# Optimization experiments

Hardware: AMD Instinct MI355X
Metric: run time of the kernel (lower is better)

Reference implementation:

```python
import jax, jax.numpy as jnp
import numpy as np

SR = 44100
PRE_EMPH = 0.97
FRAME_LEN = int(0.02 * SR)      # 882
FRAME_HOP = FRAME_LEN // 2      # 441
N_FFT = 2048
EPS = 1e-10


def setup_inputs() -> dict:
    key = jax.random.key(0)
    k1, k2 = jax.random.split(key)
    waveform = jax.random.normal(k1, (16, 441000), dtype=jnp.float32)
    # librosa mel filterbank is a fixed nonnegative (n_mels, n_fft//2+1) matrix;
    # a random surrogate keeps the math (dense matmul) identical.
    mel_filters = jax.random.uniform(k2, (60, N_FFT // 2 + 1), dtype=jnp.float32)
    return {"waveform": waveform, "mel_filters": mel_filters}


def _mfdwc(waveform, mel_filters):
    dt = waveform.dtype
    # pre-emphasis: y[0]=x[0], y[t]=x[t]-0.97*x[t-1]
    emph = jnp.concatenate(
        [waveform[:, :1], waveform[:, 1:] - PRE_EMPH * waveform[:, :-1]], axis=1)
    L = emph.shape[1]
    n_frames = 1 + (L - FRAME_LEN) // FRAME_HOP  # static
    idx = jnp.arange(n_frames)[:, None] * FRAME_HOP + jnp.arange(FRAME_LEN)[None, :]
    frames = emph[:, idx]                                   # (B, T, 882)
    window = jnp.asarray(np.hamming(FRAME_LEN), dtype=dt)   # (882,)
    windowed = frames * window
    spec = jnp.fft.rfft(windowed, n=N_FFT, axis=-1)         # (B, T, 1025) complex
    power = jnp.real(spec) ** 2 + jnp.imag(spec) ** 2       # |FFT|^2
    mel = jnp.einsum('mf,btf->btm', mel_filters, power)     # (B, T, 60)
    logmel = jnp.log(mel + EPS)
    # 1-level Haar DWT along mel axis (pywt convention, even length):
    # cA = (x_even + x_odd)/sqrt(2), cD = (x_even - x_odd)/sqrt(2)
    sq2 = jnp.sqrt(jnp.asarray(2.0, dt))
    x_even, x_odd = logmel[..., 0::2], logmel[..., 1::2]
    cA = (x_even + x_odd) / sq2                             # (B, T, 30)
    cD = (x_even - x_odd) / sq2                             # (B, T, 30)
    # delta (window=3, edge-padded): d[t] = a[clamp(t+1)] - a[clamp(t-1)]
    fwd = jnp.concatenate([cA[:, 1:], cA[:, -1:]], axis=1)
    bwd = jnp.concatenate([cA[:, :1], cA[:, :-1]], axis=1)
    delta = fwd - bwd
    feats = jnp.concatenate([cA, delta, cD], axis=-1)       # (B, T, 90)
    mean = jnp.mean(feats, axis=1)
    std = jnp.std(feats, axis=1, ddof=1)                    # torch.std unbiased
    return jnp.concatenate([mean, std], axis=1)             # (B, 180)


def reference(waveform, mel_filters):
    return _mfdwc(waveform, mel_filters)
```

## Files before the change

### kernel.cpp

```cpp
#include <hip/hip_runtime.h>
#include <hip/hip_bf16.h>
#include <math.h>

#define FRAME_LEN 882
#define FRAME_HOP 441
#define NFFT 2048
#define NFRAMES 999
#define NBATCH 16
#define NMEL 60
#define WAVE_LEN 441000
#define PRE_EMPH 0.97f
#define EPS 1e-10f
#define NROWS (NBATCH * NFRAMES)
#define NPANEL 999
#define KPAD 1056
#define NKC 33
#define PANEL_ELEMS (NKC * 512)
#define PANEL_BYTES (PANEL_ELEMS * 2)
#define PI_F 3.14159265358979323846f

#define PADI(i) ((i) + ((i) >> 4))

__device__ __forceinline__ int frag_off(int m, int k) {
  return ((k >> 5) * 512) | (((k >> 3) & 3) * 128) | (m * 8) | (k & 7);
}

typedef float vf2 __attribute__((ext_vector_type(2)));
__device__ __forceinline__ vf2 mkv(float x, float y){ vf2 r; r.x = x; r.y = y; return r; }
__device__ __forceinline__ vf2 cmul(vf2 a, vf2 b){ return a.xx * b + mkv(-a.y, a.y) * b.yx; }
__device__ __forceinline__ vf2 rotni(vf2 z){ return mkv(z.y, -z.x); }

__device__ __forceinline__ void dif_group16(vf2* x, vf2 t1, bool zerohi) {
  const vf2 C81 = mkv(0.9238795325f, -0.3826834324f);
  const vf2 C82 = mkv(0.7071067812f, -0.7071067812f);
  const vf2 C83 = mkv(0.3826834324f, -0.9238795325f);
  vf2 w0 = t1, w1 = cmul(t1, C81), w2 = cmul(t1, C82), w3 = cmul(t1, C83);
  vf2 ws1[8] = {w0, w1, w2, w3, rotni(w0), rotni(w1), rotni(w2), rotni(w3)};
  if (zerohi) {
#pragma unroll
    for (int k = 0; k < 8; ++k) x[k + 8] = cmul(x[k], ws1[k]);
  } else {
#pragma unroll
    for (int k = 0; k < 8; ++k) {
      vf2 u = x[k], v = x[k + 8];
      x[k] = u + v;
      x[k + 8] = cmul(u - v, ws1[k]);
    }
  }
  vf2 t2 = cmul(t1, t1);
  vf2 v1 = cmul(t2, C82);
  vf2 ws2[4] = {t2, v1, rotni(t2), rotni(v1)};
#pragma unroll
  for (int h = 0; h < 2; ++h) {
#pragma unroll
    for (int k = 0; k < 4; ++k) {
      vf2 u = x[h*8 + k], v = x[h*8 + k + 4];
      x[h*8 + k] = u + v;
      x[h*8 + k + 4] = cmul(u - v, ws2[k]);
    }
  }
  vf2 t4 = cmul(t2, t2);
  vf2 t4r = rotni(t4);
#pragma unroll
  for (int h = 0; h < 4; ++h) {
    vf2 a = x[h*4 + 0], b = x[h*4 + 2];
    x[h*4 + 0] = a + b; x[h*4 + 2] = cmul(a - b, t4);
    a = x[h*4 + 1]; b = x[h*4 + 3];
    x[h*4 + 1] = a + b; x[h*4 + 3] = cmul(a - b, t4r);
  }
  vf2 t8 = cmul(t4, t4);
#pragma unroll
  for (int j = 0; j < 8; ++j) {
    vf2 a = x[2*j], b = x[2*j + 1];
    x[2*j] = a + b; x[2*j + 1] = cmul(a - b, t8);
  }
}

__device__ __forceinline__ void dif8(vf2* y) {
  const vf2 c1 = mkv(0.7071067812f, -0.7071067812f);
  const vf2 c3 = mkv(-0.7071067812f, -0.7071067812f);
  vf2 u, v;
  u=y[0]; v=y[4]; y[0]=u+v; y[4]=u-v;
  u=y[1]; v=y[5]; y[1]=u+v; y[5]=cmul(u-v, c1);
  u=y[2]; v=y[6]; y[2]=u+v; y[6]=rotni(u-v);
  u=y[3]; v=y[7]; y[3]=u+v; y[7]=cmul(u-v, c3);
  u=y[0]; v=y[2]; y[0]=u+v; y[2]=u-v;
  u=y[1]; v=y[3]; y[1]=u+v; y[3]=rotni(u-v);
  u=y[4]; v=y[6]; y[4]=u+v; y[6]=u-v;
  u=y[5]; v=y[7]; y[5]=u+v; y[7]=rotni(u-v);
  u=y[0]; v=y[1]; y[0]=u+v; y[1]=u-v;
  u=y[2]; v=y[3]; y[2]=u+v; y[3]=u-v;
  u=y[4]; v=y[5]; y[4]=u+v; y[5]=u-v;
  u=y[6]; v=y[7]; y[6]=u+v; y[7]=u-v;
}

__global__ __launch_bounds__(256) void fft_pow_kernel(
    const float* __restrict__ wav, const float* __restrict__ filt,
    __hip_bfloat16* __restrict__ powrF, __hip_bfloat16* __restrict__ filtbF)
{
  __shared__ vf2 lds2[2][NFFT + (NFFT >> 4)];
  const int id = blockIdx.x;

  if (id >= 4000) {
    const int mm = id - 4000;
    __hip_bfloat16* qp = filtbF + (size_t)(mm >> 4) * PANEL_ELEMS;
    const int m = mm & 15;
    for (int k = threadIdx.x; k < KPAD; k += 256) {
      float v = (mm < NMEL && k < 1025) ? filt[mm * 1025 + k] : 0.f;
      qp[frag_off(m, k)] = __float2bfloat16(v);
    }
    return;
  }

  const int t   = threadIdx.x;
  const int fid = t >> 7;
  const int tt  = t & 127;
  vf2* lds = lds2[fid];

  const int P  = id * 2 + fid;
  const int b  = P & 15;
  const int t0 = 2 * (P >> 4), t1f = t0 + 1;
  const bool has1 = (t1f < NFRAMES);
  const float* w = wav + (size_t)b * WAVE_LEN;
  const int s0 = t0 * FRAME_HOP;
  int s1 = t1f * FRAME_HOP;
  if (s1 > WAVE_LEN - FRAME_LEN) s1 = WAVE_LEN - FRAME_LEN;

  vf2 x[16];
  {
    float sB, cB, sD, cD;
    __sincosf(6.283185307179586f * (float)tt / 881.0f, &sB, &cB);
    __sincosf(6.283185307179586f * 128.0f / 881.0f, &sD, &cD);
    vf2 cur  = mkv(cB, sB);
    vf2 step = mkv(cD, sD);
#pragma unroll
    for (int k = 0; k < 7; ++k) {
      int i = k * 128 + tt;
      float v1 = 0.f, v2 = 0.f;
      if (i < FRAME_LEN) {
        float win = 0.54f - 0.46f * cur.x;
        int s = s0 + i;
        float e1 = (s > 0) ? (w[s] - PRE_EMPH * w[s - 1]) : w[s];
        v1 = e1 * win;
        int ss = s1 + i;
        v2 = (w[ss] - PRE_EMPH * w[ss - 1]) * win;
      }
      x[k] = mkv(v1, v2);
      cur = cmul(cur, step);
    }
#pragma unroll
    for (int k = 7; k < 16; ++k) x[k] = mkv(0.f, 0.f);
  }

  {
    float sA, cA;
    __sincosf(-PI_F * (float)tt / 1024.0f, &sA, &cA);
    dif_group16(x, mkv(cA, sA), true);
  }
#pragma unroll
  for (int k = 0; k < 16; ++k) lds[PADI(k * 128 + tt)] = x[k];
  __syncthreads();

  {
    const int Q = tt >> 3, r = tt & 7;
    const int base = Q * 128 + r;
#pragma unroll
    for (int k = 0; k < 16; ++k) x[k] = lds[PADI(base + k * 8)];
    float sA, cA;
    __sincosf(-PI_F * (float)r / 64.0f, &sA, &cA);
    dif_group16(x, mkv(cA, sA), false);
#pragma unroll
    for (int k = 0; k < 16; ++k) lds[PADI(base + k * 8)] = x[k];
  }
  __syncthreads();

  {
    vf2 ya[8], yb[8];
#pragma unroll
    for (int j = 0; j < 8; ++j) {
      ya[j] = lds[PADI(16 * tt + j)];
      yb[j] = lds[PADI(16 * tt + 8 + j)];
    }
    dif8(ya);
    dif8(yb);
    __syncthreads();
    const int r7 = (int)(__brev((unsigned)tt) >> 25);
    const int RA[8] = {0, 8, 4, 12, 2, 10, 6, 14};
    const int RB[8] = {1, 9, 5, 13, 3, 11, 7, 15};
#pragma unroll
    for (int j = 0; j < 8; ++j) {
      lds[PADI(RA[j] * 128 + r7)] = ya[j];
      lds[PADI(RB[j] * 128 + r7)] = yb[j];
    }
  }
  __syncthreads();

  const int r0g = b * NFRAMES + t0;
  const int r1g = r0g + 1;
  __hip_bfloat16* q0 = powrF + (size_t)(r0g >> 4) * PANEL_ELEMS;
  const int m0 = r0g & 15;
  __hip_bfloat16* q1 = powrF + (size_t)(r1g >> 4) * PANEL_ELEMS;
  const int m1 = r1g & 15;
#pragma unroll
  for (int c = 0; c < 8; ++c) {
    int f = c * 128 + tt;
    int mir = (NFFT - f) & (NFFT - 1);
    vf2 z = lds[PADI(f)];
    vf2 y = lds[PADI(mir)];
    float f1r = z.x + y.x, f1i = z.y - y.y;
    float f2r = z.y + y.y, f2i = y.x - z.x;
    float pw1 = 0.25f * (f1r * f1r + f1i * f1i);
    float pw2 = 0.25f * (f2r * f2r + f2i * f2i);
    q0[frag_off(m0, f)] = __float2bfloat16(pw1);
    if (has1) q1[frag_off(m1, f)] = __float2bfloat16(pw2);
  }
  if (tt == 0) {
    vf2 z = lds[PADI(1024)];
    q0[frag_off(m0, 1024)] = __float2bfloat16(z.x * z.x);
    if (has1) q1[frag_off(m1, 1024)] = __float2bfloat16(z.y * z.y);
  }
  if (tt < KPAD - 1025) {
    int f = 1025 + tt;
    q0[frag_off(m0, f)] = __float2bfloat16(0.f);
    if (has1) q1[frag_off(m1, f)] = __float2bfloat16(0.f);
  }
}

typedef __attribute__((ext_vector_type(8))) short short8x;
typedef __attribute__((ext_vector_type(4))) float float4x;

#define PPB 2

__global__ __launch_bounds__(256) void melgemm_kernel(
    const __hip_bfloat16* __restrict__ powrF,
    const __hip_bfloat16* __restrict__ filtbF,
    float* __restrict__ logmelT)
{
  __shared__ __hip_bfloat16 As[2][PANEL_ELEMS];
  const int tid  = threadIdx.x;
  const int wave = tid >> 6, lane = tid & 63;
  const int p0 = blockIdx.x * PPB;

  auto stage = [&](int buf, int p) {
    const unsigned char* src =
        (const unsigned char*)(powrF + (size_t)p * PANEL_ELEMS);
    unsigned char* dst = (unsigned char*)As[buf];
#pragma unroll
    for (int r = 0; r < 9; ++r) {
      const int off = r * 4096 + tid * 16;
      if (off < PANEL_BYTES) {
        __builtin_amdgcn_global_load_lds(
            (const __attribute__((address_space(1))) unsigned int*)(src + off),
            (__attribute__((address_space(3))) unsigned int*)(dst + off),
            16, 0, 0);
      }
    }
  };

  stage(0, p0);

  short8x Breg[NKC];
  {
    const __hip_bfloat16* pB = filtbF + (size_t)wave * PANEL_ELEMS + lane * 8;
#pragma unroll
    for (int kc = 0; kc < NKC; ++kc)
      Breg[kc] = *(const short8x*)(pB + kc * 512);
  }

  __syncthreads();

  const int mel  = wave * 16 + (lane & 15);
  const int rsub = (lane >> 4) * 4;

  for (int i = 0; i < PPB; ++i) {
    const int p = p0 + i;
    if (p >= NPANEL) break;
    const bool more = (i + 1 < PPB) && (p + 1 < NPANEL);
    if (more) stage((i + 1) & 1, p + 1);

    const __hip_bfloat16* A = As[i & 1];
    float4x acc0 = {0.f, 0.f, 0.f, 0.f};
    float4x acc1 = {0.f, 0.f, 0.f, 0.f};
#pragma unroll
    for (int kc = 0; kc < 16; ++kc) {
      short8x a0 = *(const short8x*)(&A[kc * 512 + lane * 8]);
      short8x a1 = *(const short8x*)(&A[(kc + 16) * 512 + lane * 8]);
      acc0 = __builtin_amdgcn_mfma_f32_16x16x32_bf16(a0, Breg[kc], acc0, 0, 0, 0);
      acc1 = __builtin_amdgcn_mfma_f32_16x16x32_bf16(a1, Breg[kc + 16], acc1, 0, 0, 0);
    }
    {
      short8x a = *(const short8x*)(&A[32 * 512 + lane * 8]);
      acc0 = __builtin_amdgcn_mfma_f32_16x16x32_bf16(a, Breg[32], acc0, 0, 0, 0);
    }

    if (mel < NMEL) {
#pragma unroll
      for (int reg = 0; reg < 4; ++reg) {
        int row = p * 16 + rsub + reg;
        float vv = acc0[reg] + acc1[reg];
        logmelT[(size_t)mel * NROWS + row] = __logf(vv + EPS);
      }
    }
    if (more) __syncthreads();
  }
}

__global__ __launch_bounds__(256) void stats_kernel(
    const float* __restrict__ lmT, float* __restrict__ out)
{
  __shared__ float red[4];
  const int j   = blockIdx.x;
  const int b   = blockIdx.y;
  const int tid = threadIdx.x;
  const int base = b * NFRAMES;
  const float inv_sq2 = 0.7071067811865475f;
  const bool v3 = (tid < NFRAMES - 768);

  float f0, f1, f2, f3;
  if (j < 30) {
    const float* e = lmT + (size_t)(2 * j) * NROWS + base;
    const float* o = lmT + (size_t)(2 * j + 1) * NROWS + base;
    f0 = (e[tid]       + o[tid])       * inv_sq2;
    f1 = (e[tid + 256] + o[tid + 256]) * inv_sq2;
    f2 = (e[tid + 512] + o[tid + 512]) * inv_sq2;
    f3 = v3 ? (e[tid + 768] + o[tid + 768]) * inv_sq2 : 0.f;
  } else if (j < 60) {
    const int m = j - 30;
    const float* e = lmT + (size_t)(2 * m) * NROWS + base;
    const float* o = lmT + (size_t)(2 * m + 1) * NROWS + base;
    auto dl = [&](int t) -> float {
      int tp = (t + 1 > NFRAMES - 1) ? (NFRAMES - 1) : (t + 1);
      int tm = (t - 1 < 0) ? 0 : (t - 1);
      return ((e[tp] + o[tp]) - (e[tm] + o[tm])) * inv_sq2;
    };
    f0 = dl(tid);
    f1 = dl(tid + 256);
    f2 = dl(tid + 512);
    f3 = v3 ? dl(tid + 768) : 0.f;
  } else {
    const int m = j - 60;
    const float* e = lmT + (size_t)(2 * m) * NROWS + base;
    const float* o = lmT + (size_t)(2 * m + 1) * NROWS + base;
    f0 = (e[tid]       - o[tid])       * inv_sq2;
    f1 = (e[tid + 256] - o[tid + 256]) * inv_sq2;
    f2 = (e[tid + 512] - o[tid + 512]) * inv_sq2;
    f3 = v3 ? (e[tid + 768] - o[tid + 768]) * inv_sq2 : 0.f;
  }

  float s = f0 + f1 + f2 + f3;
  for (int o2 = 32; o2 > 0; o2 >>= 1) s += __shfl_xor(s, o2, 64);
  if ((tid & 63) == 0) red[tid >> 6] = s;
  __syncthreads();
  float mean = (red[0] + red[1] + red[2] + red[3]) / (float)NFRAMES;
  __syncthreads();

  float d0 = f0 - mean, d1 = f1 - mean, d2 = f2 - mean;
  float d3 = v3 ? (f3 - mean) : 0.f;
  float s2 = d0 * d0 + d1 * d1 + d2 * d2 + d3 * d3;
  for (int o2 = 32; o2 > 0; o2 >>= 1) s2 += __shfl_xor(s2, o2, 64);
  if ((tid & 63) == 0) red[tid >> 6] = s2;
  __syncthreads();
  float var = (red[0] + red[1] + red[2] + red[3]) / (float)(NFRAMES - 1);

  if (tid == 0) {
    out[b * 180 + j]      = mean;
    out[b * 180 + 90 + j] = sqrtf(var);
  }
}

extern "C" void kernel_launch(void* const* d_in, const int* in_sizes, int n_in,
                              void* d_out, int out_size, void* d_ws, size_t ws_size,
                              hipStream_t stream) {
  const float* wav  = (const float*)d_in[0];
  const float* filt = (const float*)d_in[1];
  float* out = (float*)d_out;

  unsigned char* ws = (unsigned char*)d_ws;
  __hip_bfloat16* powrF  = (__hip_bfloat16*)(ws);
  size_t off = (size_t)NPANEL * PANEL_ELEMS * 2;
  __hip_bfloat16* filtbF = (__hip_bfloat16*)(ws + off);
  off += (size_t)4 * PANEL_ELEMS * 2;
  float* logmelT = (float*)(ws + off);

  fft_pow_kernel<<<4064, 256, 0, stream>>>(wav, filt, powrF, filtbF);
  melgemm_kernel<<<500, 256, 0, stream>>>(powrF, filtbF, logmelT);
  stats_kernel<<<dim3(90, NBATCH), 256, 0, stream>>>(logmelT, out);
}
```

Before: 115.5 us.

## Restructure 2048-point FFT as radix-8 with 256 threads per frame pair

The FFT kernel moves from 128 threads per frame pair (two pairs per block), with two radix-16 passes and a radix-8 pass, to 256 threads per pair: three radix-8 passes plus a final radix-4. Per-thread register arrays shrink from 16 to 8 complex values, and launch bounds request 8 blocks per SM, so occupancy should rise. The cost is one extra LDS round trip and barrier per FFT and twice as many blocks.

```diff
diff --git a/kernel.cpp b/kernel.cpp
--- a/kernel.cpp
+++ b/kernel.cpp
@@ -30,79 +30,55 @@
 __device__ __forceinline__ vf2 cmul(vf2 a, vf2 b){ return a.xx * b + mkv(-a.y, a.y) * b.yx; }
 __device__ __forceinline__ vf2 rotni(vf2 z){ return mkv(z.y, -z.x); }
 
-__device__ __forceinline__ void dif_group16(vf2* x, vf2 t1, bool zerohi) {
-  const vf2 C81 = mkv(0.9238795325f, -0.3826834324f);
+__device__ __forceinline__ void dif_group8(vf2* x, vf2 t1, bool zerohi) {
   const vf2 C82 = mkv(0.7071067812f, -0.7071067812f);
-  const vf2 C83 = mkv(0.3826834324f, -0.9238795325f);
-  vf2 w0 = t1, w1 = cmul(t1, C81), w2 = cmul(t1, C82), w3 = cmul(t1, C83);
-  vf2 ws1[8] = {w0, w1, w2, w3, rotni(w0), rotni(w1), rotni(w2), rotni(w3)};
+  vf2 w0 = t1, w1 = cmul(t1, C82);
+  vf2 ws1[4] = {w0, w1, rotni(w0), rotni(w1)};
   if (zerohi) {
 #pragma unroll
-    for (int k = 0; k < 8; ++k) x[k + 8] = cmul(x[k], ws1[k]);
+    for (int k = 0; k < 4; ++k) x[k + 4] = cmul(x[k], ws1[k]);
   } else {
 #pragma unroll
-    for (int k = 0; k < 8; ++k) {
-      vf2 u = x[k], v = x[k + 8];
+    for (int k = 0; k < 4; ++k) {
+      vf2 u = x[k], v = x[k + 4];
       x[k] = u + v;
-      x[k + 8] = cmul(u - v, ws1[k]);
+      x[k + 4] = cmul(u - v, ws1[k]);
     }
   }
   vf2 t2 = cmul(t1, t1);
-  vf2 v1 = cmul(t2, C82);
-  vf2 ws2[4] = {t2, v1, rotni(t2), rotni(v1)};
+  vf2 t2r = rotni(t2);
 #pragma unroll
   for (int h = 0; h < 2; ++h) {
-#pragma unroll
-    for (int k = 0; k < 4; ++k) {
-      vf2 u = x[h*8 + k], v = x[h*8 + k + 4];
-      x[h*8 + k] = u + v;
-      x[h*8 + k + 4] = cmul(u - v, ws2[k]);
-    }
+    vf2 u = x[h*4 + 0], v = x[h*4 + 2];
+    x[h*4 + 0] = u + v; x[h*4 + 2] = cmul(u - v, t2);
+    u = x[h*4 + 1]; v = x[h*4 + 3];
+    x[h*4 + 1] = u + v; x[h*4 + 3] = cmul(u - v, t2r);
   }
   vf2 t4 = cmul(t2, t2);
-  vf2 t4r = rotni(t4);
-#pragma unroll
-  for (int h = 0; h < 4; ++h) {
-    vf2 a = x[h*4 + 0], b = x[h*4 + 2];
-    x[h*4 + 0] = a + b; x[h*4 + 2] = cmul(a - b, t4);
-    a = x[h*4 + 1]; b = x[h*4 + 3];
-    x[h*4 + 1] = a + b; x[h*4 + 3] = cmul(a - b, t4r);
-  }
-  vf2 t8 = cmul(t4, t4);
-#pragma unroll
-  for (int j = 0; j < 8; ++j) {
-    vf2 a = x[2*j], b = x[2*j + 1];
-    x[2*j] = a + b; x[2*j + 1] = cmul(a - b, t8);
-  }
-}
-
-__device__ __forceinline__ void dif8(vf2* y) {
-  const vf2 c1 = mkv(0.7071067812f, -0.7071067812f);
-  const vf2 c3 = mkv(-0.7071067812f, -0.7071067812f);
+#pragma unroll
+  for (int j = 0; j < 4; ++j) {
+    vf2 u = x[2*j], v = x[2*j + 1];
+    x[2*j] = u + v; x[2*j + 1] = cmul(u - v, t4);
+  }
+}
+
+__device__ __forceinline__ void dif4(vf2* y) {
   vf2 u, v;
-  u=y[0]; v=y[4]; y[0]=u+v; y[4]=u-v;
-  u=y[1]; v=y[5]; y[1]=u+v; y[5]=cmul(u-v, c1);
-  u=y[2]; v=y[6]; y[2]=u+v; y[6]=rotni(u-v);
-  u=y[3]; v=y[7]; y[3]=u+v; y[7]=cmul(u-v, c3);
   u=y[0]; v=y[2]; y[0]=u+v; y[2]=u-v;
   u=y[1]; v=y[3]; y[1]=u+v; y[3]=rotni(u-v);
-  u=y[4]; v=y[6]; y[4]=u+v; y[6]=u-v;
-  u=y[5]; v=y[7]; y[5]=u+v; y[7]=rotni(u-v);
   u=y[0]; v=y[1]; y[0]=u+v; y[1]=u-v;
   u=y[2]; v=y[3]; y[2]=u+v; y[3]=u-v;
-  u=y[4]; v=y[5]; y[4]=u+v; y[5]=u-v;
-  u=y[6]; v=y[7]; y[6]=u+v; y[7]=u-v;
-}
-
-__global__ __launch_bounds__(256) void fft_pow_kernel(
+}
+
+__global__ __launch_bounds__(256, 8) void fft_pow_kernel(
     const float* __restrict__ wav, const float* __restrict__ filt,
     __hip_bfloat16* __restrict__ powrF, __hip_bfloat16* __restrict__ filtbF)
 {
-  __shared__ vf2 lds2[2][NFFT + (NFFT >> 4)];
+  __shared__ vf2 lds[NFFT + (NFFT >> 4)];
   const int id = blockIdx.x;
 
-  if (id >= 4000) {
-    const int mm = id - 4000;
+  if (id >= 8000) {
+    const int mm = id - 8000;
     __hip_bfloat16* qp = filtbF + (size_t)(mm >> 4) * PANEL_ELEMS;
     const int m = mm & 15;
     for (int k = threadIdx.x; k < KPAD; k += 256) {
@@ -112,12 +88,9 @@
     return;
   }
 
-  const int t   = threadIdx.x;
-  const int fid = t >> 7;
-  const int tt  = t & 127;
-  vf2* lds = lds2[fid];
-
-  const int P  = id * 2 + fid;
+  const int tt = threadIdx.x;
+
+  const int P  = id;
   const int b  = P & 15;
   const int t0 = 2 * (P >> 4), t1f = t0 + 1;
   const bool has1 = (t1f < NFRAMES);
@@ -126,16 +99,16 @@
   int s1 = t1f * FRAME_HOP;
   if (s1 > WAVE_LEN - FRAME_LEN) s1 = WAVE_LEN - FRAME_LEN;
 
-  vf2 x[16];
+  vf2 x[8];
   {
     float sB, cB, sD, cD;
     __sincosf(6.283185307179586f * (float)tt / 881.0f, &sB, &cB);
-    __sincosf(6.283185307179586f * 128.0f / 881.0f, &sD, &cD);
+    __sincosf(6.283185307179586f * 256.0f / 881.0f, &sD, &cD);
     vf2 cur  = mkv(cB, sB);
     vf2 step = mkv(cD, sD);
 #pragma unroll
-    for (int k = 0; k < 7; ++k) {
-      int i = k * 128 + tt;
+    for (int k = 0; k < 4; ++k) {
+      int i = k * 256 + tt;
       float v1 = 0.f, v2 = 0.f;
       if (i < FRAME_LEN) {
         float win = 0.54f - 0.46f * cur.x;
@@ -149,48 +122,61 @@
       cur = cmul(cur, step);
     }
 #pragma unroll
-    for (int k = 7; k < 16; ++k) x[k] = mkv(0.f, 0.f);
-  }
-
-  {
-    float sA, cA;
-    __sincosf(-PI_F * (float)tt / 1024.0f, &sA, &cA);
-    dif_group16(x, mkv(cA, sA), true);
-  }
-#pragma unroll
-  for (int k = 0; k < 16; ++k) lds[PADI(k * 128 + tt)] = x[k];
-  __syncthreads();
-
-  {
-    const int Q = tt >> 3, r = tt & 7;
-    const int base = Q * 128 + r;
-#pragma unroll
-    for (int k = 0; k < 16; ++k) x[k] = lds[PADI(base + k * 8)];
-    float sA, cA;
-    __sincosf(-PI_F * (float)r / 64.0f, &sA, &cA);
-    dif_group16(x, mkv(cA, sA), false);
-#pragma unroll
-    for (int k = 0; k < 16; ++k) lds[PADI(base + k * 8)] = x[k];
-  }
-  __syncthreads();
-
-  {
-    vf2 ya[8], yb[8];
-#pragma unroll
-    for (int j = 0; j < 8; ++j) {
-      ya[j] = lds[PADI(16 * tt + j)];
-      yb[j] = lds[PADI(16 * tt + 8 + j)];
-    }
-    dif8(ya);
-    dif8(yb);
+    for (int k = 4; k < 8; ++k) x[k] = mkv(0.f, 0.f);
+  }
+
+  {
+    float s_, c_;
+    __sincosf(-PI_F * (float)tt / 1024.0f, &s_, &c_);
+    dif_group8(x, mkv(c_, s_), true);
+  }
+#pragma unroll
+  for (int k = 0; k < 8; ++k) lds[PADI(k * 256 + tt)] = x[k];
+  __syncthreads();
+
+  {
+    const int Q = tt >> 5, r = tt & 31;
+    const int base = Q * 256 + r;
+#pragma unroll
+    for (int k = 0; k < 8; ++k) x[k] = lds[PADI(base + k * 32)];
+    float s_, c_;
+    __sincosf(-PI_F * (float)r / 128.0f, &s_, &c_);
+    dif_group8(x, mkv(c_, s_), false);
+#pragma unroll
+    for (int k = 0; k < 8; ++k) lds[PADI(base + k * 32)] = x[k];
+  }
+  __syncthreads();
+
+  {
+    const int q = tt >> 2, r2 = tt & 3;
+    const int base = q * 32 + r2;
+#pragma unroll
+    for (int k = 0; k < 8; ++k) x[k] = lds[PADI(base + k * 4)];
+    float s_, c_;
+    __sincosf(-PI_F * (float)r2 / 16.0f, &s_, &c_);
+    dif_group8(x, mkv(c_, s_), false);
+#pragma unroll
+    for (int k = 0; k < 8; ++k) lds[PADI(base + k * 4)] = x[k];
+  }
+  __syncthreads();
+
+  {
+    vf2 ya[4], yb[4];
+#pragma unroll
+    for (int j = 0; j < 4; ++j) {
+      ya[j] = lds[PADI(8 * tt + j)];
+      yb[j] = lds[PADI(8 * tt + 4 + j)];
+    }
+    dif4(ya);
+    dif4(yb);
     __syncthreads();
-    const int r7 = (int)(__brev((unsigned)tt) >> 25);
-    const int RA[8] = {0, 8, 4, 12, 2, 10, 6, 14};
-    const int RB[8] = {1, 9, 5, 13, 3, 11, 7, 15};
-#pragma unroll
-    for (int j = 0; j < 8; ++j) {
-      lds[PADI(RA[j] * 128 + r7)] = ya[j];
-      lds[PADI(RB[j] * 128 + r7)] = yb[j];
+    const int r8 = (int)(__brev((unsigned)tt) >> 24);
+    const int RA[4] = {0, 4, 2, 6};
+    const int RB[4] = {1, 5, 3, 7};
+#pragma unroll
+    for (int j = 0; j < 4; ++j) {
+      lds[PADI(RA[j] * 256 + r8)] = ya[j];
+      lds[PADI(RB[j] * 256 + r8)] = yb[j];
     }
   }
   __syncthreads();
@@ -202,8 +188,8 @@
   __hip_bfloat16* q1 = powrF + (size_t)(r1g >> 4) * PANEL_ELEMS;
   const int m1 = r1g & 15;
 #pragma unroll
-  for (int c = 0; c < 8; ++c) {
-    int f = c * 128 + tt;
+  for (int c = 0; c < 4; ++c) {
+    int f = c * 256 + tt;
     int mir = (NFFT - f) & (NFFT - 1);
     vf2 z = lds[PADI(f)];
     vf2 y = lds[PADI(mir)];
@@ -382,7 +368,7 @@
   off += (size_t)4 * PANEL_ELEMS * 2;
   float* logmelT = (float*)(ws + off);
 
-  fft_pow_kernel<<<4064, 256, 0, stream>>>(wav, filt, powrF, filtbF);
+  fft_pow_kernel<<<8064, 256, 0, stream>>>(wav, filt, powrF, filtbF);
   melgemm_kernel<<<500, 256, 0, stream>>>(powrF, filtbF, logmelT);
   stats_kernel<<<dim3(90, NBATCH), 256, 0, stream>>>(logmelT, out);
 }
```

After: 115.6 us. Within noise of the previous version (+0.1%).
